# Performance work log

Hardware: AMD Instinct MI355X
Metric: run time of the kernel (lower is better)

The kernel has to match this reference:

```python
import jax, jax.numpy as jnp
import numpy as np

E = 2_000_000   # edges
N = 200_000     # nodes
E_DIM = 128     # edge feature dim
G_DIM = 256     # global/graph feature dim
B = 1024        # number of graphs (batch.max()+1)
EPS = 1e-6      # torch_scatter scatter_std eps


def setup_inputs() -> dict:
    key = jax.random.key(0)
    k1, k2, k3, k4 = jax.random.split(key, 4)
    e = jax.random.normal(k1, (E, E_DIM), dtype=jnp.float32)
    e_index = jax.random.randint(k2, (2, E), 0, N, dtype=jnp.int64)
    batch = jnp.sort(jax.random.randint(k3, (N,), 0, B, dtype=jnp.int64))
    fc_w = jax.random.normal(k4, (E_DIM * 4, G_DIM), dtype=jnp.float32) * 0.02
    fc_b = jnp.zeros((G_DIM,), dtype=jnp.float32)
    return {"e_index": e_index, "e": e, "batch": batch, "fc_w": fc_w, "fc_b": fc_b}


def reference(e_index, e, batch, fc_w, fc_b):
    # graph id per edge (via target node of each edge)
    e_batch = batch[e_index[1]]  # [E]

    count = jax.ops.segment_sum(jnp.ones((e.shape[0],), e.dtype), e_batch,
                                num_segments=B)[:, None]  # [B, 1]
    s = jax.ops.segment_sum(e, e_batch, num_segments=B)    # [B, D]

    # scatter(reduce='mean'): empty segments -> 0 (divide by clamped count)
    mean = s / jnp.maximum(count, 1.0)

    # scatter min/max: torch_scatter fills empty segments with 0
    mn = jax.ops.segment_min(e, e_batch, num_segments=B)
    mx = jax.ops.segment_max(e, e_batch, num_segments=B)
    empty = count == 0.0
    mn = jnp.where(empty, 0.0, mn)
    mx = jnp.where(empty, 0.0, mx)

    # scatter_std (unbiased, matches torch_scatter composite):
    # std = sqrt(sum((x - mean)^2) / (clamp(count-1, 1) + eps))
    diff = e - mean[e_batch]                               # [E, D]
    var_sum = jax.ops.segment_sum(diff * diff, e_batch, num_segments=B)
    denom = jnp.maximum(count - 1.0, 1.0) + EPS
    std = jnp.sqrt(var_sum / denom)

    g = jnp.concatenate([mean, mn, mx, std], axis=1)       # [B, 4D]
    return g @ fc_w + fc_b                                 # [B, G_DIM]
```

## Files before the change

### kernel.cpp

```cpp
#include <hip/hip_runtime.h>
#include <math.h>

#define DIMS 128
#define GD 256
#define MAXB 1024
#define NSLOT 8
#define PARTS 4
#define NBLK 256
#define SCH 8192

typedef float vfloat4 __attribute__((ext_vector_type(4)));

__device__ __forceinline__ float4 ldnt(const float* p) {
    vfloat4 v = __builtin_nontemporal_load(reinterpret_cast<const vfloat4*>(p));
    return make_float4(v.x, v.y, v.z, v.w);
}
__device__ __forceinline__ float4 f4_add(float4 a, float4 b) {
    return make_float4(a.x + b.x, a.y + b.y, a.z + b.z, a.w + b.w);
}
__device__ __forceinline__ float4 f4_min(float4 a, float4 b) {
    return make_float4(fminf(a.x, b.x), fminf(a.y, b.y), fminf(a.z, b.z), fminf(a.w, b.w));
}
__device__ __forceinline__ float4 f4_max(float4 a, float4 b) {
    return make_float4(fmaxf(a.x, b.x), fmaxf(a.y, b.y), fmaxf(a.z, b.z), fmaxf(a.w, b.w));
}

template <int OP>
__device__ __forceinline__ float4 comb(float4 a, float4 b) {
    if (OP == 0) return f4_add(a, b);
    if (OP == 1) return f4_min(a, b);
    return f4_max(a, b);
}

template <int OP>
__device__ __forceinline__ float4 slot_reduce(float4 v, float4* red) {
    int t = threadIdx.x;
    __syncthreads();
    red[t] = v;
    __syncthreads();
    for (int off = 128; off >= 32; off >>= 1) {
        if (t < off) red[t] = comb<OP>(red[t], red[t + off]);
        __syncthreads();
    }
    return red[t & 31];
}

#define ACC(v) do { \
    sm = f4_add(sm, v); \
    sq = f4_add(sq, make_float4((v).x*(v).x, (v).y*(v).y, (v).z*(v).z, (v).w*(v).w)); \
    mn = f4_min(mn, v); mx = f4_max(mx, v); } while (0)

__global__ void __launch_bounds__(256)
hist2_kernel(const int* __restrict__ e_index, const int* __restrict__ batch,
             int E, int* __restrict__ hist2, unsigned short* __restrict__ eb) {
    __shared__ int lh[MAXB];
    for (int i = threadIdx.x; i < MAXB; i += 256) lh[i] = 0;
    __syncthreads();
    int b = blockIdx.x;
    int CH = (E + NBLK - 1) / NBLK;
    int lo = b * CH;
    int hi = min(E, lo + CH);
    for (int j = lo + threadIdx.x; j < hi; j += 256) {
        int node = e_index[E + j];
        int g = batch[node];
        eb[j] = (unsigned short)g;
        atomicAdd(&lh[g], 1);
    }
    __syncthreads();
    for (int i = threadIdx.x; i < MAXB; i += 256)
        hist2[(size_t)b * MAXB + i] = lh[i];
}

__global__ void __launch_bounds__(256)
colscan_kernel(int* __restrict__ hist2, int* __restrict__ count) {
    int g = blockIdx.x;
    int t = threadIdx.x;
    int v = hist2[(size_t)t * MAXB + g];
    __shared__ int ws[256];
    ws[t] = v;
    __syncthreads();
    for (int d = 1; d < 256; d <<= 1) {
        int x = (t >= d) ? ws[t - d] : 0;
        __syncthreads();
        ws[t] += x;
        __syncthreads();
    }
    hist2[(size_t)t * MAXB + g] = ws[t] - v;
    if (t == 255) count[g] = ws[255];
}

__global__ void __launch_bounds__(256)
scatter_kernel(const unsigned short* __restrict__ eb, const int* __restrict__ hist2,
               const int* __restrict__ count, int E,
               int* __restrict__ perm, int* __restrict__ offs) {
    __shared__ int lhist[MAXB];
    __shared__ int lofs[MAXB];
    __shared__ int lcur[MAXB];
    __shared__ int lbase[MAXB];
    __shared__ int ws[256];
    __shared__ int bin[SCH];
    int b = blockIdx.x;
    int t = threadIdx.x;
    int CH = (E + NBLK - 1) / NBLK;
    int lo = b * CH;
    int hi = min(E, lo + CH);
    int base = t * 4;

    int g0 = count[base + 0], g1 = count[base + 1], g2 = count[base + 2], g3 = count[base + 3];
    int gsum = g0 + g1 + g2 + g3;
    ws[t] = gsum;
    __syncthreads();
    for (int d = 1; d < 256; d <<= 1) {
        int x = (t >= d) ? ws[t - d] : 0;
        __syncthreads();
        ws[t] += x;
        __syncthreads();
    }
    int gexcl = ws[t] - gsum;
    int ob0 = gexcl, ob1 = gexcl + g0, ob2 = gexcl + g0 + g1, ob3 = gexcl + g0 + g1 + g2;
    if (b == 0) {
        offs[base + 0] = ob0; offs[base + 1] = ob1;
        offs[base + 2] = ob2; offs[base + 3] = ob3;
    }
    lbase[base + 0] = ob0 + hist2[(size_t)b * MAXB + base + 0];
    lbase[base + 1] = ob1 + hist2[(size_t)b * MAXB + base + 1];
    lbase[base + 2] = ob2 + hist2[(size_t)b * MAXB + base + 2];
    lbase[base + 3] = ob3 + hist2[(size_t)b * MAXB + base + 3];
    lhist[base + 0] = 0; lhist[base + 1] = 0; lhist[base + 2] = 0; lhist[base + 3] = 0;
    __syncthreads();

    for (int j = lo + t; j < hi; j += 256) atomicAdd(&lhist[eb[j]], 1);
    __syncthreads();

    int c0 = lhist[base + 0], c1 = lhist[base + 1], c2 = lhist[base + 2], c3 = lhist[base + 3];
    int s0 = c0 + c1 + c2 + c3;
    ws[t] = s0;
    __syncthreads();
    for (int d = 1; d < 256; d <<= 1) {
        int x = (t >= d) ? ws[t - d] : 0;
        __syncthreads();
        ws[t] += x;
        __syncthreads();
    }
    int excl = ws[t] - s0;
    lofs[base + 0] = excl;
    lofs[base + 1] = excl + c0;
    lofs[base + 2] = excl + c0 + c1;
    lofs[base + 3] = excl + c0 + c1 + c2;
    lcur[base + 0] = excl;
    lcur[base + 1] = excl + c0;
    lcur[base + 2] = excl + c0 + c1;
    lcur[base + 3] = excl + c0 + c1 + c2;
    __syncthreads();

    for (int j = lo + t; j < hi; j += 256) {
        int g = eb[j];
        int r = atomicAdd(&lcur[g], 1);
        bin[r] = j;
    }
    __syncthreads();

    int grp = t >> 3, sub = t & 7;
    for (int g = grp; g < MAXB; g += 32) {
        int sfrom = lofs[g];
        int n = lcur[g] - sfrom;
        int dst = lbase[g];
        for (int k = sub; k < n; k += 8)
            perm[dst + k] = bin[sfrom + k];
    }
}

__global__ void __launch_bounds__(256)
reduce_kernel(const float* __restrict__ e, const int* __restrict__ perm,
              const int* __restrict__ offs, const int* __restrict__ count,
              float* __restrict__ pbuf) {
    int bid = blockIdx.x;
    int g = bid >> 2;
    int p = bid & 3;
    int start = offs[g];
    int cnt = count[g];
    int chunk = (cnt + PARTS - 1) / PARTS;
    int base = start + p * chunk;
    int cnt_p = cnt - p * chunk;
    if (cnt_p > chunk) cnt_p = chunk;
    if (cnt_p < 0) cnt_p = 0;
    const int* pp = perm + base;

    int c = threadIdx.x & 31;
    int s = threadIdx.x >> 5;

    float4 sm = make_float4(0.f, 0.f, 0.f, 0.f);
    float4 sq = make_float4(0.f, 0.f, 0.f, 0.f);
    float4 mn = make_float4(INFINITY, INFINITY, INFINITY, INFINITY);
    float4 mx = make_float4(-INFINITY, -INFINITY, -INFINITY, -INFINITY);

    int i = s;
    if (i + 3 * NSLOT < cnt_p) {
        int ia0 = pp[i], ia1 = pp[i + NSLOT], ia2 = pp[i + 2 * NSLOT], ia3 = pp[i + 3 * NSLOT];
        while (true) {
            int ni = i + 4 * NSLOT;
            int na0 = 0, na1 = 0, na2 = 0, na3 = 0;
            bool nok = (ni + 3 * NSLOT < cnt_p);
            if (nok) { na0 = pp[ni]; na1 = pp[ni + NSLOT]; na2 = pp[ni + 2 * NSLOT]; na3 = pp[ni + 3 * NSLOT]; }
            float4 v0 = ldnt(e + (size_t)ia0 * DIMS + c * 4);
            float4 v1 = ldnt(e + (size_t)ia1 * DIMS + c * 4);
            float4 v2 = ldnt(e + (size_t)ia2 * DIMS + c * 4);
            float4 v3 = ldnt(e + (size_t)ia3 * DIMS + c * 4);
            ACC(v0); ACC(v1); ACC(v2); ACC(v3);
            i = ni;
            if (!nok) break;
            ia0 = na0; ia1 = na1; ia2 = na2; ia3 = na3;
        }
    }
    for (; i < cnt_p; i += NSLOT) {
        int r = pp[i];
        float4 v = ldnt(e + (size_t)r * DIMS + c * 4);
        ACC(v);
    }

    __shared__ float4 red[256];
    float4 smr = slot_reduce<0>(sm, red);
    float4 mnr = slot_reduce<1>(mn, red);
    float4 mxr = slot_reduce<2>(mx, red);
    float4 sqr = slot_reduce<0>(sq, red);

    if (threadIdx.x < 32) {
        float* row = pbuf + (size_t)bid * (4 * DIMS);
        int d0 = c * 4;
        *reinterpret_cast<float4*>(row + 0 * DIMS + d0) = smr;
        *reinterpret_cast<float4*>(row + 1 * DIMS + d0) = mnr;
        *reinterpret_cast<float4*>(row + 2 * DIMS + d0) = mxr;
        *reinterpret_cast<float4*>(row + 3 * DIMS + d0) = sqr;
    }
}

__global__ void __launch_bounds__(256)
gemm_kernel(const float* __restrict__ pbuf, const int* __restrict__ count,
            const float* __restrict__ w, const float* __restrict__ bias,
            float* __restrict__ out, int B) {
    __shared__ float gl[8 * 512];
    int r0 = blockIdx.x * 8;
    int t = threadIdx.x;
#pragma unroll
    for (int q = 0; q < 4; ++q) {
        int pair = q * 256 + t;
        int r = pair >> 7;
        int d = pair & 127;
        int g = r0 + r;
        float sm = 0.f, sq = 0.f, mnv = INFINITY, mxv = -INFINITY;
        int cnt = 0;
        if (g < B) {
            cnt = count[g];
            const float* pb = pbuf + (size_t)g * PARTS * 512;
#pragma unroll
            for (int p = 0; p < PARTS; ++p) {
                const float* row = pb + p * 512;
                sm += row[d];
                mnv = fminf(mnv, row[128 + d]);
                mxv = fmaxf(mxv, row[256 + d]);
                sq += row[384 + d];
            }
        }
        float fc = (float)cnt;
        float fcm = fmaxf(fc, 1.0f);
        float mean = sm / fcm;
        float vs = fmaxf(sq - sm * mean, 0.f);
        float sd = sqrtf(vs / (fmaxf(fc - 1.0f, 1.0f) + 1e-6f));
        if (cnt == 0) { mnv = 0.f; mxv = 0.f; }
        gl[r * 512 + 0 * 128 + d] = mean;
        gl[r * 512 + 1 * 128 + d] = mnv;
        gl[r * 512 + 2 * 128 + d] = mxv;
        gl[r * 512 + 3 * 128 + d] = sd;
    }
    __syncthreads();

    int col = t;
    float acc[8];
    float bv = bias[col];
#pragma unroll
    for (int r = 0; r < 8; ++r) acc[r] = bv;
#pragma unroll 4
    for (int k = 0; k < 512; ++k) {
        float wv = w[k * GD + col];
#pragma unroll
        for (int r = 0; r < 8; ++r) acc[r] += gl[r * 512 + k] * wv;
    }
#pragma unroll
    for (int r = 0; r < 8; ++r) {
        int rr = r0 + r;
        if (rr < B) out[(size_t)rr * GD + col] = acc[r];
    }
}

extern "C" void kernel_launch(void* const* d_in, const int* in_sizes, int n_in,
                              void* d_out, int out_size, void* d_ws, size_t ws_size,
                              hipStream_t stream) {
    const int*   e_index = (const int*)d_in[0];
    const float* e       = (const float*)d_in[1];
    const int*   batch   = (const int*)d_in[2];
    const float* fc_w    = (const float*)d_in[3];
    const float* fc_b    = (const float*)d_in[4];
    float* out = (float*)d_out;

    int E = in_sizes[1] / DIMS;
    int B = out_size / GD;

    int* hist2 = (int*)d_ws;
    int* count = hist2 + (size_t)NBLK * MAXB;
    int* offs  = count + MAXB;
    unsigned short* eb = (unsigned short*)(offs + MAXB);
    int* perm  = (int*)(eb + (((size_t)E + 1) & ~(size_t)1));
    float* pbuf = (float*)(perm + E);

    hist2_kernel<<<NBLK, 256, 0, stream>>>(e_index, batch, E, hist2, eb);
    colscan_kernel<<<MAXB, 256, 0, stream>>>(hist2, count);
    scatter_kernel<<<NBLK, 256, 0, stream>>>(eb, hist2, count, E, perm, offs);
    reduce_kernel<<<B * PARTS, 256, 0, stream>>>(e, perm, offs, count, pbuf);
    gemm_kernel<<<(B + 7) / 8, 256, 0, stream>>>(pbuf, count, fc_w, fc_b, out, B);
}
```

Before: 267.0 us.

## Reuse raw histogram in scatter, one block per graph, finalize stats in reduce

The scatter kernel now reads per-block raw histograms written by hist2, using a separate scanned buffer, instead of recounting edges with shared atomics. The reduce kernel drops the 4-way split per graph and uses one block per graph. It replaces the multi-barrier tree reduction with a single shared-memory stage and computes mean/min/max/std directly, so the GEMM kernel only loads the finished features. This removes a pass over eb and several barriers, but each block now handles about four times as many edges, which lowers parallelism in the bandwidth-bound gather. The reduce grid is also fixed at MAXB rather than B.

```diff
diff --git a/kernel.cpp b/kernel.cpp
--- a/kernel.cpp
+++ b/kernel.cpp
@@ -5,7 +5,6 @@
 #define GD 256
 #define MAXB 1024
 #define NSLOT 8
-#define PARTS 4
 #define NBLK 256
 #define SCH 8192
 
@@ -23,26 +22,6 @@
 }
 __device__ __forceinline__ float4 f4_max(float4 a, float4 b) {
     return make_float4(fmaxf(a.x, b.x), fmaxf(a.y, b.y), fmaxf(a.z, b.z), fmaxf(a.w, b.w));
-}
-
-template <int OP>
-__device__ __forceinline__ float4 comb(float4 a, float4 b) {
-    if (OP == 0) return f4_add(a, b);
-    if (OP == 1) return f4_min(a, b);
-    return f4_max(a, b);
-}
-
-template <int OP>
-__device__ __forceinline__ float4 slot_reduce(float4 v, float4* red) {
-    int t = threadIdx.x;
-    __syncthreads();
-    red[t] = v;
-    __syncthreads();
-    for (int off = 128; off >= 32; off >>= 1) {
-        if (t < off) red[t] = comb<OP>(red[t], red[t + off]);
-        __syncthreads();
-    }
-    return red[t & 31];
 }
 
 #define ACC(v) do { \
@@ -52,7 +31,7 @@
 
 __global__ void __launch_bounds__(256)
 hist2_kernel(const int* __restrict__ e_index, const int* __restrict__ batch,
-             int E, int* __restrict__ hist2, unsigned short* __restrict__ eb) {
+             int E, int* __restrict__ hist2r, unsigned short* __restrict__ eb) {
     __shared__ int lh[MAXB];
     for (int i = threadIdx.x; i < MAXB; i += 256) lh[i] = 0;
     __syncthreads();
@@ -68,14 +47,15 @@
     }
     __syncthreads();
     for (int i = threadIdx.x; i < MAXB; i += 256)
-        hist2[(size_t)b * MAXB + i] = lh[i];
-}
-
-__global__ void __launch_bounds__(256)
-colscan_kernel(int* __restrict__ hist2, int* __restrict__ count) {
+        hist2r[(size_t)b * MAXB + i] = lh[i];
+}
+
+__global__ void __launch_bounds__(256)
+colscan_kernel(const int* __restrict__ hist2r, int* __restrict__ hist2s,
+               int* __restrict__ count) {
     int g = blockIdx.x;
     int t = threadIdx.x;
-    int v = hist2[(size_t)t * MAXB + g];
+    int v = hist2r[(size_t)t * MAXB + g];
     __shared__ int ws[256];
     ws[t] = v;
     __syncthreads();
@@ -85,15 +65,14 @@
         ws[t] += x;
         __syncthreads();
     }
-    hist2[(size_t)t * MAXB + g] = ws[t] - v;
+    hist2s[(size_t)t * MAXB + g] = ws[t] - v;
     if (t == 255) count[g] = ws[255];
 }
 
 __global__ void __launch_bounds__(256)
-scatter_kernel(const unsigned short* __restrict__ eb, const int* __restrict__ hist2,
-               const int* __restrict__ count, int E,
+scatter_kernel(const unsigned short* __restrict__ eb, const int* __restrict__ hist2r,
+               const int* __restrict__ hist2s, const int* __restrict__ count, int E,
                int* __restrict__ perm, int* __restrict__ offs) {
-    __shared__ int lhist[MAXB];
     __shared__ int lofs[MAXB];
     __shared__ int lcur[MAXB];
     __shared__ int lbase[MAXB];
@@ -122,17 +101,16 @@
         offs[base + 0] = ob0; offs[base + 1] = ob1;
         offs[base + 2] = ob2; offs[base + 3] = ob3;
     }
-    lbase[base + 0] = ob0 + hist2[(size_t)b * MAXB + base + 0];
-    lbase[base + 1] = ob1 + hist2[(size_t)b * MAXB + base + 1];
-    lbase[base + 2] = ob2 + hist2[(size_t)b * MAXB + base + 2];
-    lbase[base + 3] = ob3 + hist2[(size_t)b * MAXB + base + 3];
-    lhist[base + 0] = 0; lhist[base + 1] = 0; lhist[base + 2] = 0; lhist[base + 3] = 0;
-    __syncthreads();
-
-    for (int j = lo + t; j < hi; j += 256) atomicAdd(&lhist[eb[j]], 1);
-    __syncthreads();
-
-    int c0 = lhist[base + 0], c1 = lhist[base + 1], c2 = lhist[base + 2], c3 = lhist[base + 3];
+    lbase[base + 0] = ob0 + hist2s[(size_t)b * MAXB + base + 0];
+    lbase[base + 1] = ob1 + hist2s[(size_t)b * MAXB + base + 1];
+    lbase[base + 2] = ob2 + hist2s[(size_t)b * MAXB + base + 2];
+    lbase[base + 3] = ob3 + hist2s[(size_t)b * MAXB + base + 3];
+    __syncthreads();
+
+    int c0 = hist2r[(size_t)b * MAXB + base + 0];
+    int c1 = hist2r[(size_t)b * MAXB + base + 1];
+    int c2 = hist2r[(size_t)b * MAXB + base + 2];
+    int c3 = hist2r[(size_t)b * MAXB + base + 3];
     int s0 = c0 + c1 + c2 + c3;
     ws[t] = s0;
     __syncthreads();
@@ -173,18 +151,11 @@
 __global__ void __launch_bounds__(256)
 reduce_kernel(const float* __restrict__ e, const int* __restrict__ perm,
               const int* __restrict__ offs, const int* __restrict__ count,
-              float* __restrict__ pbuf) {
-    int bid = blockIdx.x;
-    int g = bid >> 2;
-    int p = bid & 3;
+              float* __restrict__ gbuf) {
+    int g = blockIdx.x;
     int start = offs[g];
     int cnt = count[g];
-    int chunk = (cnt + PARTS - 1) / PARTS;
-    int base = start + p * chunk;
-    int cnt_p = cnt - p * chunk;
-    if (cnt_p > chunk) cnt_p = chunk;
-    if (cnt_p < 0) cnt_p = 0;
-    const int* pp = perm + base;
+    const int* pp = perm + start;
 
     int c = threadIdx.x & 31;
     int s = threadIdx.x >> 5;
@@ -195,12 +166,12 @@
     float4 mx = make_float4(-INFINITY, -INFINITY, -INFINITY, -INFINITY);
 
     int i = s;
-    if (i + 3 * NSLOT < cnt_p) {
+    if (i + 3 * NSLOT < cnt) {
         int ia0 = pp[i], ia1 = pp[i + NSLOT], ia2 = pp[i + 2 * NSLOT], ia3 = pp[i + 3 * NSLOT];
         while (true) {
             int ni = i + 4 * NSLOT;
             int na0 = 0, na1 = 0, na2 = 0, na3 = 0;
-            bool nok = (ni + 3 * NSLOT < cnt_p);
+            bool nok = (ni + 3 * NSLOT < cnt);
             if (nok) { na0 = pp[ni]; na1 = pp[ni + NSLOT]; na2 = pp[ni + 2 * NSLOT]; na3 = pp[ni + 3 * NSLOT]; }
             float4 v0 = ldnt(e + (size_t)ia0 * DIMS + c * 4);
             float4 v1 = ldnt(e + (size_t)ia1 * DIMS + c * 4);
@@ -212,65 +183,65 @@
             ia0 = na0; ia1 = na1; ia2 = na2; ia3 = na3;
         }
     }
-    for (; i < cnt_p; i += NSLOT) {
+    for (; i < cnt; i += NSLOT) {
         int r = pp[i];
         float4 v = ldnt(e + (size_t)r * DIMS + c * 4);
         ACC(v);
     }
 
-    __shared__ float4 red[256];
-    float4 smr = slot_reduce<0>(sm, red);
-    float4 mnr = slot_reduce<1>(mn, red);
-    float4 mxr = slot_reduce<2>(mx, red);
-    float4 sqr = slot_reduce<0>(sq, red);
-
-    if (threadIdx.x < 32) {
-        float* row = pbuf + (size_t)bid * (4 * DIMS);
-        int d0 = c * 4;
-        *reinterpret_cast<float4*>(row + 0 * DIMS + d0) = smr;
-        *reinterpret_cast<float4*>(row + 1 * DIMS + d0) = mnr;
-        *reinterpret_cast<float4*>(row + 2 * DIMS + d0) = mxr;
-        *reinterpret_cast<float4*>(row + 3 * DIMS + d0) = sqr;
-    }
-}
-
-__global__ void __launch_bounds__(256)
-gemm_kernel(const float* __restrict__ pbuf, const int* __restrict__ count,
-            const float* __restrict__ w, const float* __restrict__ bias,
-            float* __restrict__ out, int B) {
-    __shared__ float gl[8 * 512];
-    int r0 = blockIdx.x * 8;
-    int t = threadIdx.x;
-#pragma unroll
-    for (int q = 0; q < 4; ++q) {
-        int pair = q * 256 + t;
-        int r = pair >> 7;
-        int d = pair & 127;
-        int g = r0 + r;
-        float sm = 0.f, sq = 0.f, mnv = INFINITY, mxv = -INFINITY;
-        int cnt = 0;
-        if (g < B) {
-            cnt = count[g];
-            const float* pb = pbuf + (size_t)g * PARTS * 512;
-#pragma unroll
-            for (int p = 0; p < PARTS; ++p) {
-                const float* row = pb + p * 512;
-                sm += row[d];
-                mnv = fminf(mnv, row[128 + d]);
-                mxv = fmaxf(mxv, row[256 + d]);
-                sq += row[384 + d];
-            }
+    __shared__ float4 red[4][NSLOT][32];
+    red[0][s][c] = sm;
+    red[1][s][c] = mn;
+    red[2][s][c] = mx;
+    red[3][s][c] = sq;
+    __syncthreads();
+
+    int t = threadIdx.x;
+    if (t < 128) {
+        int stat = t >> 5;
+        int cc = t & 31;
+        float4 a = red[stat][0][cc];
+        if (stat == 1) {
+#pragma unroll
+            for (int k = 1; k < NSLOT; ++k) a = f4_min(a, red[1][k][cc]);
+        } else if (stat == 2) {
+#pragma unroll
+            for (int k = 1; k < NSLOT; ++k) a = f4_max(a, red[2][k][cc]);
+        } else {
+#pragma unroll
+            for (int k = 1; k < NSLOT; ++k) a = f4_add(a, red[stat][k][cc]);
         }
         float fc = (float)cnt;
         float fcm = fmaxf(fc, 1.0f);
-        float mean = sm / fcm;
-        float vs = fmaxf(sq - sm * mean, 0.f);
-        float sd = sqrtf(vs / (fmaxf(fc - 1.0f, 1.0f) + 1e-6f));
-        if (cnt == 0) { mnv = 0.f; mxv = 0.f; }
-        gl[r * 512 + 0 * 128 + d] = mean;
-        gl[r * 512 + 1 * 128 + d] = mnv;
-        gl[r * 512 + 2 * 128 + d] = mxv;
-        gl[r * 512 + 3 * 128 + d] = sd;
+        float4 r;
+        if (stat == 0) {
+            r = make_float4(a.x / fcm, a.y / fcm, a.z / fcm, a.w / fcm);
+        } else if (stat == 1 || stat == 2) {
+            r = (cnt == 0) ? make_float4(0.f, 0.f, 0.f, 0.f) : a;
+        } else {
+            float4 smr = red[0][0][cc];
+#pragma unroll
+            for (int k = 1; k < NSLOT; ++k) smr = f4_add(smr, red[0][k][cc]);
+            float4 mean = make_float4(smr.x / fcm, smr.y / fcm, smr.z / fcm, smr.w / fcm);
+            float denom = fmaxf(fc - 1.0f, 1.0f) + 1e-6f;
+            r = make_float4(sqrtf(fmaxf(a.x - smr.x * mean.x, 0.f) / denom),
+                            sqrtf(fmaxf(a.y - smr.y * mean.y, 0.f) / denom),
+                            sqrtf(fmaxf(a.z - smr.z * mean.z, 0.f) / denom),
+                            sqrtf(fmaxf(a.w - smr.w * mean.w, 0.f) / denom));
+        }
+        *reinterpret_cast<float4*>(gbuf + (size_t)g * 512 + stat * DIMS + cc * 4) = r;
+    }
+}
+
+__global__ void __launch_bounds__(256)
+gemm_kernel(const float* __restrict__ gbuf, const float* __restrict__ w,
+            const float* __restrict__ bias, float* __restrict__ out, int B) {
+    __shared__ float gl[8 * 512];
+    int r0 = blockIdx.x * 8;
+    int t = threadIdx.x;
+    for (int i = t; i < 8 * 512; i += 256) {
+        int r = r0 + (i >> 9);
+        gl[i] = (r < B) ? gbuf[(size_t)r0 * 512 + i] : 0.f;
     }
     __syncthreads();
 
@@ -305,16 +276,17 @@
     int E = in_sizes[1] / DIMS;
     int B = out_size / GD;
 
-    int* hist2 = (int*)d_ws;
-    int* count = hist2 + (size_t)NBLK * MAXB;
-    int* offs  = count + MAXB;
+    int* hist2r = (int*)d_ws;
+    int* hist2s = hist2r + (size_t)NBLK * MAXB;
+    int* count  = hist2s + (size_t)NBLK * MAXB;
+    int* offs   = count + MAXB;
     unsigned short* eb = (unsigned short*)(offs + MAXB);
-    int* perm  = (int*)(eb + (((size_t)E + 1) & ~(size_t)1));
-    float* pbuf = (float*)(perm + E);
-
-    hist2_kernel<<<NBLK, 256, 0, stream>>>(e_index, batch, E, hist2, eb);
-    colscan_kernel<<<MAXB, 256, 0, stream>>>(hist2, count);
-    scatter_kernel<<<NBLK, 256, 0, stream>>>(eb, hist2, count, E, perm, offs);
-    reduce_kernel<<<B * PARTS, 256, 0, stream>>>(e, perm, offs, count, pbuf);
-    gemm_kernel<<<(B + 7) / 8, 256, 0, stream>>>(pbuf, count, fc_w, fc_b, out, B);
-}
+    int* perm   = (int*)(eb + (((size_t)E + 1) & ~(size_t)1));
+    float* gbuf = (float*)(perm + E);
+
+    hist2_kernel<<<NBLK, 256, 0, stream>>>(e_index, batch, E, hist2r, eb);
+    colscan_kernel<<<MAXB, 256, 0, stream>>>(hist2r, hist2s, count);
+    scatter_kernel<<<NBLK, 256, 0, stream>>>(eb, hist2r, hist2s, count, E, perm, offs);
+    reduce_kernel<<<MAXB, 256, 0, stream>>>(e, perm, offs, count, gbuf);
+    gemm_kernel<<<(B + 7) / 8, 256, 0, stream>>>(gbuf, fc_w, fc_b, out, B);
+}
```

New measurement: 262.5 us, median of 2. Within noise of the previous version (-1.7%).
